# Kernel tuning notes

Hardware: AMD Instinct MI355X
Metric: run time of the kernel (lower is better)

Reference implementation:

```python
import jax, jax.numpy as jnp
import numpy as np

NUM_HEADS = 16

def setup_inputs() -> dict:
    key = jax.random.key(0)
    k1, k2, k3 = jax.random.split(key, 3)
    B, T, C = 2, 2048, 1024
    x = jax.random.normal(k1, (B, T, C), dtype=jnp.float32)
    w_qkv = jax.random.normal(k2, (3 * C, C), dtype=jnp.float32) * (C ** -0.5)
    w_out = jax.random.normal(k3, (C, C), dtype=jnp.float32) * (C ** -0.5)
    b_out = jnp.zeros((C,), dtype=jnp.float32)
    return {"x": x, "w_qkv": w_qkv, "w_out": w_out, "b_out": b_out}

def reference(x, w_qkv, w_out, b_out):
    B, T, C = x.shape
    H = NUM_HEADS
    dh = C // H
    scale = 1.0 / jnp.sqrt(jnp.float32(dh))
    # fused qkv projection (torch Linear: x @ W^T), no bias
    qkv = jnp.einsum('btc,dc->btd', x, w_qkv)  # [B,T,3C]
    q, k, v = jnp.split(qkv, 3, axis=-1)
    # [B,H,T,dh]
    q = q.reshape(B, T, H, dh).transpose(0, 2, 1, 3)
    k = k.reshape(B, T, H, dh).transpose(0, 2, 1, 3)
    v = v.reshape(B, T, H, dh).transpose(0, 2, 1, 3)
    att = jnp.einsum('bhqd,bhkd->bhqk', q, k) * scale  # [B,H,T,T]
    causal = jnp.tril(jnp.ones((T, T), dtype=bool))
    att = jnp.where(causal[None, None, :, :], att, jnp.float32(-jnp.inf))
    att = jax.nn.softmax(att, axis=-1)
    y = jnp.einsum('bhqk,bhkd->bhqd', att, v)  # [B,H,T,dh]
    y = y.transpose(0, 2, 1, 3).reshape(B, T, C)
    y = jnp.einsum('btc,dc->btd', y, w_out) + b_out
    return y
```

## Files before the change

### kernel.cpp

```cpp
#include <hip/hip_runtime.h>
#include <hip/hip_bf16.h>
#include <math.h>

typedef __bf16 bf16x8 __attribute__((ext_vector_type(8)));
typedef __bf16 bf16x4 __attribute__((ext_vector_type(4)));
typedef float  f32x4  __attribute__((ext_vector_type(4)));

#define MFMA16(A, B, C) __builtin_amdgcn_mfma_f32_16x16x32_bf16(A, B, C, 0, 0, 0)

__device__ __forceinline__ void gload_lds16(const void* g, void* l) {
  __builtin_amdgcn_global_load_lds((const __attribute__((address_space(1))) void*)g,
                                   (__attribute__((address_space(3))) void*)l, 16, 0, 0);
}

__device__ __forceinline__ float exp2_fast(float x) {
  float r; asm("v_exp_f32 %0, %1" : "=v"(r) : "v"(x)); return r;
}

__device__ __forceinline__ unsigned lds_off(const void* p) {
  return (unsigned)(size_t)(const __attribute__((address_space(3))) void*)p;
}

__device__ __forceinline__ bf16x4 ds_tr16(unsigned byte_addr) {
  bf16x4 r;
  asm volatile("ds_read_b64_tr_b16 %0, %1" : "=v"(r) : "v"(byte_addr));
  return r;
}

__global__ __launch_bounds__(256) void cvt_all(const float* __restrict__ x,
                                               const float* __restrict__ wq,
                                               const float* __restrict__ wo,
                                               __bf16* __restrict__ xb,
                                               __bf16* __restrict__ wqb,
                                               __bf16* __restrict__ wob) {
  int i = (blockIdx.x * 256 + threadIdx.x) * 8;
  const float* s;
  __bf16*      d;
  if (i < 4194304) {
    s = x; d = xb;
  } else if (i < 4194304 + 3145728) {
    i -= 4194304; s = wq; d = wqb;
  } else {
    i -= 4194304 + 3145728; s = wo; d = wob;
  }
  const float4 a = *(const float4*)(s + i);
  const float4 b = *(const float4*)(s + i + 4);
  bf16x8 v;
  v[0] = (__bf16)a.x; v[1] = (__bf16)a.y; v[2] = (__bf16)a.z; v[3] = (__bf16)a.w;
  v[4] = (__bf16)b.x; v[5] = (__bf16)b.y; v[6] = (__bf16)b.z; v[7] = (__bf16)b.w;
  *(bf16x8*)(d + i) = v;
}

template <bool BIAS, typename CT>
__global__ __launch_bounds__(256) void gemm_bt(const __bf16* __restrict__ A,
                                               const __bf16* __restrict__ B,
                                               const float* __restrict__ bias,
                                               CT* __restrict__ C, int M, int N, int K) {
  __shared__ alignas(16) __bf16 As[2][128 * 32];
  __shared__ alignas(16) __bf16 Bs[2][128 * 32];

  const int tid  = threadIdx.x;
  const int lane = tid & 63;
  const int wv   = tid >> 6;
  const int wr   = wv >> 1, wc = wv & 1;
  const int row0 = blockIdx.y * 128;
  const int col0 = blockIdx.x * 128;
  const int NT   = K >> 5;

  f32x4 acc[4][4] = {};

  auto stage = [&](int buf, int kt) {
    const int k0 = kt << 5;
#pragma unroll
    for (int i = 0; i < 2; ++i) {
      const int n    = i * 256 + tid;
      const int row  = n >> 2;
      const int slot = (n & 3) ^ ((row >> 1) & 3);
      gload_lds16(A + (size_t)(row0 + row) * K + (k0 + slot * 8),
                  &As[buf][(i * 256 + wv * 64) * 8]);
    }
#pragma unroll
    for (int i = 0; i < 2; ++i) {
      const int n    = i * 256 + tid;
      const int row  = n >> 2;
      const int slot = (n & 3) ^ ((row >> 1) & 3);
      gload_lds16(B + (size_t)(col0 + row) * K + (k0 + slot * 8),
                  &Bs[buf][(i * 256 + wv * 64) * 8]);
    }
  };

  stage(0, 0);
  __syncthreads();
  int cur = 0;
  for (int kt = 0; kt < NT; ++kt) {
    if (kt + 1 < NT) stage(cur ^ 1, kt + 1);

    bf16x8 af[4], bfr[4];
#pragma unroll
    for (int m = 0; m < 4; ++m) {
      const int row  = wr * 64 + m * 16 + (lane & 15);
      const int slot = (lane >> 4) ^ ((row >> 1) & 3);
      af[m] = *(const bf16x8*)&As[cur][row * 32 + slot * 8];
    }
#pragma unroll
    for (int n = 0; n < 4; ++n) {
      const int row  = wc * 64 + n * 16 + (lane & 15);
      const int slot = (lane >> 4) ^ ((row >> 1) & 3);
      bfr[n] = *(const bf16x8*)&Bs[cur][row * 32 + slot * 8];
    }
#pragma unroll
    for (int m = 0; m < 4; ++m)
#pragma unroll
      for (int n = 0; n < 4; ++n) acc[m][n] = MFMA16(af[m], bfr[n], acc[m][n]);

    __syncthreads();
    cur ^= 1;
  }

#pragma unroll
  for (int n = 0; n < 4; ++n) {
    const int   col = col0 + wc * 64 + n * 16 + (lane & 15);
    const float bv  = BIAS ? bias[col] : 0.0f;
#pragma unroll
    for (int m = 0; m < 4; ++m) {
      const int rbase = row0 + wr * 64 + m * 16 + ((lane >> 4) << 2);
#pragma unroll
      for (int r = 0; r < 4; ++r)
        C[(size_t)(rbase + r) * N + col] = (CT)(acc[m][n][r] + bv);
    }
  }
}

__global__ __launch_bounds__(256) void attn_fwd(const __bf16* __restrict__ qkv,
                                                __bf16* __restrict__ yo) {
  __shared__ alignas(16) __bf16 Ks[2][64 * 64];
  __shared__ alignas(16) __bf16 Vs[2][64 * 64];

  const int tid  = threadIdx.x;
  const int lane = tid & 63;
  const int ql   = lane & 15;
  const int g    = lane >> 4;
  const int wv   = tid >> 6;

  const int bid = blockIdx.x;
  const int qt  = 31 - (bid >> 5);
  const int bh  = bid & 31;
  const int b   = bh >> 4;
  const int h   = bh & 15;
  const int q0  = qt * 64;
  const int qw  = q0 + wv * 16;
  const int NT  = qt + 1;

  const size_t  rs = 3072;
  const __bf16* Qg = qkv + (size_t)b * 2048 * rs + h * 64;
  const __bf16* Kg = Qg + 1024;
  const __bf16* Vg = Qg + 2048;

  const int slotK = ((tid & 7) ^ ((tid >> 3) & 7)) << 3;
  const int keyV  = ((tid >> 5) << 2) + ((tid >> 1) & 3);
  const int dV    = (((tid >> 3) & 3) << 4) + ((tid & 1) << 3);
  const __bf16* kP0 = Kg + (size_t)(tid >> 3) * rs + slotK;
  const __bf16* kP1 = kP0 + 32 * rs;
  const __bf16* vP0 = Vg + (size_t)keyV * rs + dV;
  const __bf16* vP1 = vP0 + 32 * rs;
  const size_t  step = 64 * rs;

  auto stageKV = [&](int buf) {
    gload_lds16(kP0, &Ks[buf][wv * 512]);
    gload_lds16(kP1, &Ks[buf][2048 + wv * 512]);
    gload_lds16(vP0, &Vs[buf][wv * 512]);
    gload_lds16(vP1, &Vs[buf][2048 + wv * 512]);
    kP0 += step; kP1 += step; vP0 += step; vP1 += step;
  };

  bf16x8 aQ[2];
#pragma unroll
  for (int ks = 0; ks < 2; ++ks) {
    aQ[ks] = *(const bf16x8*)(Qg + (size_t)(qw + ql) * rs + ks * 32 + (g << 3));
#pragma unroll
    for (int e = 0; e < 8; ++e) aQ[ks][e] = aQ[ks][e] * (__bf16)0.125f;
  }

  bf16x8 vones;
#pragma unroll
  for (int e = 0; e < 8; ++e) vones[e] = (__bf16)1.0f;

  f32x4 o[5] = {};
  float m2 = -INFINITY;

  const float L   = 1.44269504088896f;
  const float THR = 5.5451774f;
  const unsigned vbase = lds_off(&Vs[0][0]);

  const int bidx0 = ((lane & 16) << 3) + (ql << 2);
  const int bidx1 = bidx0 + 64;

  int cur = 0;
  stageKV(0);
  __syncthreads();

  for (int t = 0; t < NT; ++t) {
    const int  k0  = t << 6;
    const bool pre = (t + 1 < NT);
    if (pre) stageKV(cur ^ 1);

    f32x4 sc[4] = {};
    __builtin_amdgcn_s_setprio(1);
#pragma unroll
    for (int n = 0; n < 4; ++n) {
#pragma unroll
      for (int ks = 0; ks < 2; ++ks) {
        const int krow = n * 16 + ql;
        const int slot = ((ks << 2) + g) ^ (krow & 7);
        bf16x8    kf   = *(const bf16x8*)&Ks[cur][krow * 64 + slot * 8];
        sc[n]          = MFMA16(kf, aQ[ks], sc[n]);
      }
    }
    __builtin_amdgcn_s_setprio(0);

    const unsigned abase = vbase + (cur ? 8192u : 0u) + (g << 10) + (ql << 3);
    bf16x4 vlo[2][4], vhi[2][4];
#pragma unroll
    for (int ks = 0; ks < 2; ++ks)
#pragma unroll
      for (int n = 0; n < 4; ++n) {
        vlo[ks][n] = ds_tr16(abase + ks * 4096 + n * 128);
        vhi[ks][n] = ds_tr16(abase + ks * 4096 + n * 128 + 512);
      }

    float s16[4][4];
    float mx = -INFINITY;
    if (t == NT - 1) {
      const int q = qw + ql;
#pragma unroll
      for (int n = 0; n < 4; ++n)
#pragma unroll
        for (int r = 0; r < 4; ++r) {
          const int k = k0 + n * 16 + (g << 2) + r;
          float     s = sc[n][r];
          if (k > q) s = -INFINITY;
          s16[n][r] = s;
          mx        = fmaxf(mx, s);
        }
    } else {
#pragma unroll
      for (int n = 0; n < 4; ++n)
#pragma unroll
        for (int r = 0; r < 4; ++r) {
          const float s = sc[n][r];
          s16[n][r]     = s;
          mx            = fmaxf(mx, s);
        }
    }
    mx = fmaxf(mx, __shfl_xor(mx, 16, 64));
    mx = fmaxf(mx, __shfl_xor(mx, 32, 64));

    if (__any(mx - m2 > THR)) {
      const float mnew = fmaxf(m2, mx);
      const float lsc  = exp2_fast((m2 - mnew) * L);
      m2               = mnew;
      float lf[4];
#pragma unroll
      for (int r = 0; r < 4; ++r)
        lf[r] = __int_as_float(__builtin_amdgcn_ds_bpermute(
            ((g << 2) + r) << 2, __float_as_int(lsc)));
#pragma unroll
      for (int n = 0; n < 5; ++n)
#pragma unroll
        for (int r = 0; r < 4; ++r) o[n][r] *= lf[r];
    }

    const float mL = m2 * L;
    int W[8];
#pragma unroll
    for (int n = 0; n < 4; ++n)
#pragma unroll
      for (int rp = 0; rp < 2; ++rp) {
        union { __bf16 h[2]; int i; } pk;
        pk.h[0]      = (__bf16)exp2_fast(__builtin_fmaf(s16[n][2 * rp], L, -mL));
        pk.h[1]      = (__bf16)exp2_fast(__builtin_fmaf(s16[n][2 * rp + 1], L, -mL));
        W[2 * n + rp] = pk.i;
      }

    union { int w[4]; bf16x8 v; } pa[2];
#pragma unroll
    for (int ks = 0; ks < 2; ++ks)
#pragma unroll
      for (int w = 0; w < 4; ++w) {
        const int idx = (w < 2) ? bidx0 : bidx1;
        const int t0  = __builtin_amdgcn_ds_bpermute(idx, W[4 * ks + (w & 1)]);
        const int t1  = __builtin_amdgcn_ds_bpermute(idx, W[4 * ks + 2 + (w & 1)]);
        pa[ks].w[w]   = (lane & 32) ? t1 : t0;
      }

    asm volatile("s_waitcnt lgkmcnt(0)");
    __builtin_amdgcn_sched_barrier(0);

    __builtin_amdgcn_s_setprio(1);
#pragma unroll
    for (int ks = 0; ks < 2; ++ks) {
#pragma unroll
      for (int n = 0; n < 4; ++n) {
        bf16x8 vf;
#pragma unroll
        for (int e = 0; e < 4; ++e) { vf[e] = vlo[ks][n][e]; vf[e + 4] = vhi[ks][n][e]; }
        o[n] = MFMA16(pa[ks].v, vf, o[n]);
      }
      o[4] = MFMA16(pa[ks].v, vones, o[4]);
    }
    __builtin_amdgcn_s_setprio(0);

    __syncthreads();
    cur ^= 1;
  }

#pragma unroll
  for (int n = 0; n < 4; ++n) {
    const int d = n * 16 + ql;
#pragma unroll
    for (int r = 0; r < 4; ++r) {
      const int q = qw + (g << 2) + r;
      yo[((size_t)b * 2048 + q) * 1024 + h * 64 + d] = (__bf16)(o[n][r] / o[4][r]);
    }
  }
}

extern "C" void kernel_launch(void* const* d_in, const int* in_sizes, int n_in, void* d_out,
                              int out_size, void* d_ws, size_t ws_size, hipStream_t stream) {
  (void)in_sizes; (void)n_in; (void)out_size; (void)ws_size;
  const float* x     = (const float*)d_in[0];
  const float* w_qkv = (const float*)d_in[1];
  const float* w_out = (const float*)d_in[2];
  const float* b_out = (const float*)d_in[3];
  float*       out   = (float*)d_out;

  __bf16* xb    = (__bf16*)d_ws;
  __bf16* wqkvb = xb + (size_t)4096 * 1024;
  __bf16* woutb = wqkvb + (size_t)3072 * 1024;
  __bf16* qkv   = woutb + (size_t)1024 * 1024;
  __bf16* yatt  = qkv + (size_t)4096 * 3072;

  cvt_all<<<4096, 256, 0, stream>>>(x, w_qkv, w_out, xb, wqkvb, woutb);

  gemm_bt<false, __bf16><<<dim3(24, 32), 256, 0, stream>>>(xb, wqkvb, nullptr, qkv,
                                                           4096, 3072, 1024);
  attn_fwd<<<1024, 256, 0, stream>>>(qkv, yatt);
  gemm_bt<true, float><<<dim3(8, 32), 256, 0, stream>>>(yatt, woutb, b_out, out,
                                                        4096, 1024, 1024);
}
```

Measured before the change: 113.2 us.

## Use two waves per attention block, each handling 32 query rows

The attention kernel drops to 128 threads (2 waves), and each wave now processes two 16-row query groups. Each K/V fragment loaded from LDS therefore feeds twice as many MFMAs, which halves LDS traffic per unit of compute. Blocks are reordered into classes that interleave long and short causal tiles to balance the load, and the V transposed reads are split into two phases to overlap with compute. The cost is higher register pressure, with launch bounds requesting 3 blocks per CU, and fewer waves available to hide latency.

```diff
diff --git a/kernel.cpp b/kernel.cpp
--- a/kernel.cpp
+++ b/kernel.cpp
@@ -131,8 +131,8 @@
   }
 }
 
-__global__ __launch_bounds__(256) void attn_fwd(const __bf16* __restrict__ qkv,
-                                                __bf16* __restrict__ yo) {
+__global__ __launch_bounds__(128, 3) void attn_fwd(const __bf16* __restrict__ qkv,
+                                                   __bf16* __restrict__ yo) {
   __shared__ alignas(16) __bf16 Ks[2][64 * 64];
   __shared__ alignas(16) __bf16 Vs[2][64 * 64];
 
@@ -142,14 +142,16 @@
   const int g    = lane >> 4;
   const int wv   = tid >> 6;
 
-  const int bid = blockIdx.x;
-  const int qt  = 31 - (bid >> 5);
-  const int bh  = bid & 31;
-  const int b   = bh >> 4;
-  const int h   = bh & 15;
-  const int q0  = qt * 64;
-  const int qw  = q0 + wv * 16;
-  const int NT  = qt + 1;
+  const int bid  = blockIdx.x;
+  const int kcls = bid >> 8;
+  const int j    = (bid >> 5) & 7;
+  const int bh   = bid & 31;
+  const int qt = (kcls == 0) ? 31 - j : (kcls == 1) ? 16 + j : (kcls == 2) ? 15 - j : j;
+  const int b  = bh >> 4;
+  const int h  = bh & 15;
+  const int q0 = qt * 64;
+  const int qw = q0 + wv * 32;
+  const int NT = qt + 1;
 
   const size_t  rs = 3072;
   const __bf16* Qg = qkv + (size_t)b * 2048 * rs + h * 64;
@@ -159,34 +161,36 @@
   const int slotK = ((tid & 7) ^ ((tid >> 3) & 7)) << 3;
   const int keyV  = ((tid >> 5) << 2) + ((tid >> 1) & 3);
   const int dV    = (((tid >> 3) & 3) << 4) + ((tid & 1) << 3);
-  const __bf16* kP0 = Kg + (size_t)(tid >> 3) * rs + slotK;
-  const __bf16* kP1 = kP0 + 32 * rs;
-  const __bf16* vP0 = Vg + (size_t)keyV * rs + dV;
-  const __bf16* vP1 = vP0 + 32 * rs;
+  const __bf16* kP = Kg + (size_t)(tid >> 3) * rs + slotK;
+  const __bf16* vP = Vg + (size_t)keyV * rs + dV;
   const size_t  step = 64 * rs;
 
   auto stageKV = [&](int buf) {
-    gload_lds16(kP0, &Ks[buf][wv * 512]);
-    gload_lds16(kP1, &Ks[buf][2048 + wv * 512]);
-    gload_lds16(vP0, &Vs[buf][wv * 512]);
-    gload_lds16(vP1, &Vs[buf][2048 + wv * 512]);
-    kP0 += step; kP1 += step; vP0 += step; vP1 += step;
+#pragma unroll
+    for (int i = 0; i < 4; ++i) {
+      gload_lds16(kP + (size_t)i * 16 * rs, &Ks[buf][i * 1024 + wv * 512]);
+      gload_lds16(vP + (size_t)i * 16 * rs, &Vs[buf][i * 1024 + wv * 512]);
+    }
+    kP += step; vP += step;
   };
 
-  bf16x8 aQ[2];
-#pragma unroll
-  for (int ks = 0; ks < 2; ++ks) {
-    aQ[ks] = *(const bf16x8*)(Qg + (size_t)(qw + ql) * rs + ks * 32 + (g << 3));
-#pragma unroll
-    for (int e = 0; e < 8; ++e) aQ[ks][e] = aQ[ks][e] * (__bf16)0.125f;
-  }
+  bf16x8 aQ[2][2];
+#pragma unroll
+  for (int qg = 0; qg < 2; ++qg)
+#pragma unroll
+    for (int ks = 0; ks < 2; ++ks) {
+      aQ[qg][ks] =
+          *(const bf16x8*)(Qg + (size_t)(qw + qg * 16 + ql) * rs + ks * 32 + (g << 3));
+#pragma unroll
+      for (int e = 0; e < 8; ++e) aQ[qg][ks][e] = aQ[qg][ks][e] * (__bf16)0.125f;
+    }
 
   bf16x8 vones;
 #pragma unroll
   for (int e = 0; e < 8; ++e) vones[e] = (__bf16)1.0f;
 
-  f32x4 o[5] = {};
-  float m2 = -INFINITY;
+  f32x4 o[2][5] = {};
+  float m2[2] = {-INFINITY, -INFINITY};
 
   const float L   = 1.44269504088896f;
   const float THR = 5.5451774f;
@@ -204,7 +208,7 @@
     const bool pre = (t + 1 < NT);
     if (pre) stageKV(cur ^ 1);
 
-    f32x4 sc[4] = {};
+    f32x4 sc[2][4] = {};
     __builtin_amdgcn_s_setprio(1);
 #pragma unroll
     for (int n = 0; n < 4; ++n) {
@@ -213,101 +217,125 @@
         const int krow = n * 16 + ql;
         const int slot = ((ks << 2) + g) ^ (krow & 7);
         bf16x8    kf   = *(const bf16x8*)&Ks[cur][krow * 64 + slot * 8];
-        sc[n]          = MFMA16(kf, aQ[ks], sc[n]);
+        sc[0][n]       = MFMA16(kf, aQ[0][ks], sc[0][n]);
+        sc[1][n]       = MFMA16(kf, aQ[1][ks], sc[1][n]);
       }
     }
     __builtin_amdgcn_s_setprio(0);
 
     const unsigned abase = vbase + (cur ? 8192u : 0u) + (g << 10) + (ql << 3);
-    bf16x4 vlo[2][4], vhi[2][4];
-#pragma unroll
-    for (int ks = 0; ks < 2; ++ks)
-#pragma unroll
-      for (int n = 0; n < 4; ++n) {
-        vlo[ks][n] = ds_tr16(abase + ks * 4096 + n * 128);
-        vhi[ks][n] = ds_tr16(abase + ks * 4096 + n * 128 + 512);
+    bf16x4 vlo0[4], vhi0[4];
+#pragma unroll
+    for (int n = 0; n < 4; ++n) {
+      vlo0[n] = ds_tr16(abase + n * 128);
+      vhi0[n] = ds_tr16(abase + n * 128 + 512);
+    }
+
+    union { int w[4]; bf16x8 v; } pa[2][2];
+    const bool diag = (t == NT - 1);
+#pragma unroll
+    for (int qg = 0; qg < 2; ++qg) {
+      const int qbase = qw + qg * 16;
+      float s16[4][4];
+      float mx = -INFINITY;
+      if (diag) {
+        const int q = qbase + ql;
+#pragma unroll
+        for (int n = 0; n < 4; ++n)
+#pragma unroll
+          for (int r = 0; r < 4; ++r) {
+            const int k = k0 + n * 16 + (g << 2) + r;
+            float     s = sc[qg][n][r];
+            if (k > q) s = -INFINITY;
+            s16[n][r] = s;
+            mx        = fmaxf(mx, s);
+          }
+      } else {
+#pragma unroll
+        for (int n = 0; n < 4; ++n)
+#pragma unroll
+          for (int r = 0; r < 4; ++r) {
+            const float s = sc[qg][n][r];
+            s16[n][r]     = s;
+            mx            = fmaxf(mx, s);
+          }
       }
-
-    float s16[4][4];
-    float mx = -INFINITY;
-    if (t == NT - 1) {
-      const int q = qw + ql;
+      mx = fmaxf(mx, __shfl_xor(mx, 16, 64));
+      mx = fmaxf(mx, __shfl_xor(mx, 32, 64));
+
+      if (__any(mx - m2[qg] > THR)) {
+        const float mnew = fmaxf(m2[qg], mx);
+        const float lsc  = exp2_fast((m2[qg] - mnew) * L);
+        m2[qg]           = mnew;
+        float lf[4];
+#pragma unroll
+        for (int r = 0; r < 4; ++r)
+          lf[r] = __int_as_float(__builtin_amdgcn_ds_bpermute(
+              ((g << 2) + r) << 2, __float_as_int(lsc)));
+#pragma unroll
+        for (int n = 0; n < 5; ++n)
+#pragma unroll
+          for (int r = 0; r < 4; ++r) o[qg][n][r] *= lf[r];
+      }
+
+      const float mL = m2[qg] * L;
+      int W[8];
 #pragma unroll
       for (int n = 0; n < 4; ++n)
 #pragma unroll
-        for (int r = 0; r < 4; ++r) {
-          const int k = k0 + n * 16 + (g << 2) + r;
-          float     s = sc[n][r];
-          if (k > q) s = -INFINITY;
-          s16[n][r] = s;
-          mx        = fmaxf(mx, s);
+        for (int rp = 0; rp < 2; ++rp) {
+          union { __bf16 hh[2]; int i; } pk;
+          pk.hh[0]       = (__bf16)exp2_fast(__builtin_fmaf(s16[n][2 * rp], L, -mL));
+          pk.hh[1]       = (__bf16)exp2_fast(__builtin_fmaf(s16[n][2 * rp + 1], L, -mL));
+          W[2 * n + rp]  = pk.i;
         }
-    } else {
-#pragma unroll
-      for (int n = 0; n < 4; ++n)
-#pragma unroll
-        for (int r = 0; r < 4; ++r) {
-          const float s = sc[n][r];
-          s16[n][r]     = s;
-          mx            = fmaxf(mx, s);
+
+#pragma unroll
+      for (int ks = 0; ks < 2; ++ks)
+#pragma unroll
+        for (int w = 0; w < 4; ++w) {
+          const int idx = (w < 2) ? bidx0 : bidx1;
+          const int t0  = __builtin_amdgcn_ds_bpermute(idx, W[4 * ks + (w & 1)]);
+          const int t1  = __builtin_amdgcn_ds_bpermute(idx, W[4 * ks + 2 + (w & 1)]);
+          pa[qg][ks].w[w] = (lane & 32) ? t1 : t0;
         }
     }
-    mx = fmaxf(mx, __shfl_xor(mx, 16, 64));
-    mx = fmaxf(mx, __shfl_xor(mx, 32, 64));
-
-    if (__any(mx - m2 > THR)) {
-      const float mnew = fmaxf(m2, mx);
-      const float lsc  = exp2_fast((m2 - mnew) * L);
-      m2               = mnew;
-      float lf[4];
-#pragma unroll
-      for (int r = 0; r < 4; ++r)
-        lf[r] = __int_as_float(__builtin_amdgcn_ds_bpermute(
-            ((g << 2) + r) << 2, __float_as_int(lsc)));
-#pragma unroll
-      for (int n = 0; n < 5; ++n)
-#pragma unroll
-        for (int r = 0; r < 4; ++r) o[n][r] *= lf[r];
-    }
-
-    const float mL = m2 * L;
-    int W[8];
-#pragma unroll
-    for (int n = 0; n < 4; ++n)
-#pragma unroll
-      for (int rp = 0; rp < 2; ++rp) {
-        union { __bf16 h[2]; int i; } pk;
-        pk.h[0]      = (__bf16)exp2_fast(__builtin_fmaf(s16[n][2 * rp], L, -mL));
-        pk.h[1]      = (__bf16)exp2_fast(__builtin_fmaf(s16[n][2 * rp + 1], L, -mL));
-        W[2 * n + rp] = pk.i;
-      }
-
-    union { int w[4]; bf16x8 v; } pa[2];
-#pragma unroll
-    for (int ks = 0; ks < 2; ++ks)
-#pragma unroll
-      for (int w = 0; w < 4; ++w) {
-        const int idx = (w < 2) ? bidx0 : bidx1;
-        const int t0  = __builtin_amdgcn_ds_bpermute(idx, W[4 * ks + (w & 1)]);
-        const int t1  = __builtin_amdgcn_ds_bpermute(idx, W[4 * ks + 2 + (w & 1)]);
-        pa[ks].w[w]   = (lane & 32) ? t1 : t0;
-      }
 
     asm volatile("s_waitcnt lgkmcnt(0)");
     __builtin_amdgcn_sched_barrier(0);
 
+    bf16x4 vlo1[4], vhi1[4];
+#pragma unroll
+    for (int n = 0; n < 4; ++n) {
+      vlo1[n] = ds_tr16(abase + 4096 + n * 128);
+      vhi1[n] = ds_tr16(abase + 4096 + n * 128 + 512);
+    }
     __builtin_amdgcn_s_setprio(1);
 #pragma unroll
-    for (int ks = 0; ks < 2; ++ks) {
-#pragma unroll
-      for (int n = 0; n < 4; ++n) {
-        bf16x8 vf;
-#pragma unroll
-        for (int e = 0; e < 4; ++e) { vf[e] = vlo[ks][n][e]; vf[e + 4] = vhi[ks][n][e]; }
-        o[n] = MFMA16(pa[ks].v, vf, o[n]);
-      }
-      o[4] = MFMA16(pa[ks].v, vones, o[4]);
-    }
+    for (int n = 0; n < 4; ++n) {
+      bf16x8 vf;
+#pragma unroll
+      for (int e = 0; e < 4; ++e) { vf[e] = vlo0[n][e]; vf[e + 4] = vhi0[n][e]; }
+      o[0][n] = MFMA16(pa[0][0].v, vf, o[0][n]);
+      o[1][n] = MFMA16(pa[1][0].v, vf, o[1][n]);
+    }
+    o[0][4] = MFMA16(pa[0][0].v, vones, o[0][4]);
+    o[1][4] = MFMA16(pa[1][0].v, vones, o[1][4]);
+    __builtin_amdgcn_s_setprio(0);
+
+    asm volatile("s_waitcnt lgkmcnt(0)");
+    __builtin_amdgcn_sched_barrier(0);
+    __builtin_amdgcn_s_setprio(1);
+#pragma unroll
+    for (int n = 0; n < 4; ++n) {
+      bf16x8 vf;
+#pragma unroll
+      for (int e = 0; e < 4; ++e) { vf[e] = vlo1[n][e]; vf[e + 4] = vhi1[n][e]; }
+      o[0][n] = MFMA16(pa[0][1].v, vf, o[0][n]);
+      o[1][n] = MFMA16(pa[1][1].v, vf, o[1][n]);
+    }
+    o[0][4] = MFMA16(pa[0][1].v, vones, o[0][4]);
+    o[1][4] = MFMA16(pa[1][1].v, vones, o[1][4]);
     __builtin_amdgcn_s_setprio(0);
 
     __syncthreads();
@@ -315,14 +343,17 @@
   }
 
 #pragma unroll
-  for (int n = 0; n < 4; ++n) {
-    const int d = n * 16 + ql;
-#pragma unroll
-    for (int r = 0; r < 4; ++r) {
-      const int q = qw + (g << 2) + r;
-      yo[((size_t)b * 2048 + q) * 1024 + h * 64 + d] = (__bf16)(o[n][r] / o[4][r]);
-    }
-  }
+  for (int qg = 0; qg < 2; ++qg)
+#pragma unroll
+    for (int n = 0; n < 4; ++n) {
+      const int d = n * 16 + ql;
+#pragma unroll
+      for (int r = 0; r < 4; ++r) {
+        const int q = qw + qg * 16 + (g << 2) + r;
+        yo[((size_t)b * 2048 + q) * 1024 + h * 64 + d] =
+            (__bf16)(o[qg][n][r] / o[qg][4][r]);
+      }
+    }
 }
 
 extern "C" void kernel_launch(void* const* d_in, const int* in_sizes, int n_in, void* d_out,
@@ -344,7 +375,7 @@
 
   gemm_bt<false, __bf16><<<dim3(24, 32), 256, 0, stream>>>(xb, wqkvb, nullptr, qkv,
                                                            4096, 3072, 1024);
-  attn_fwd<<<1024, 256, 0, stream>>>(qkv, yatt);
+  attn_fwd<<<1024, 128, 0, stream>>>(qkv, yatt);
   gemm_bt<true, float><<<dim3(8, 32), 256, 0, stream>>>(yatt, woutb, b_out, out,
                                                         4096, 1024, 1024);
 }
```

After: 125.2 us. 1.11x slower.
